# Kernel optimization log

Hardware: AMD Instinct MI355X
Metric: run time of the kernel (lower is better)

Reference implementation:

```python
import jax, jax.numpy as jnp
import numpy as np

D_MODEL = 1024
N_HEADS = 16
HEAD_DIM = D_MODEL // N_HEADS  # 64


def setup_inputs() -> dict:
    key = jax.random.key(0)
    k1, k2, k3 = jax.random.split(key, 3)
    x = jax.random.normal(k1, (2, 2048, D_MODEL), dtype=jnp.float32)
    # nn.Linear(d, 3d, bias=False): store transposed so y = x @ W
    w_qkv = jax.random.normal(k2, (D_MODEL, 3 * D_MODEL), dtype=jnp.float32) * (D_MODEL ** -0.5)
    w_proj = jax.random.normal(k3, (D_MODEL, D_MODEL), dtype=jnp.float32) * (D_MODEL ** -0.5)
    return {"x": x, "w_qkv": w_qkv, "w_proj": w_proj}


def reference(x, w_qkv, w_proj):
    b, n, _ = x.shape
    qkv = x @ w_qkv  # [b, n, 3*d_model]
    # einops 'b n (h d qkv) -> qkv b h n d': qkv axis is innermost of the split
    qkv = qkv.reshape(b, n, N_HEADS, HEAD_DIM, 3)
    q = jnp.moveaxis(qkv[..., 0], 1, 2)  # [b, h, n, d]
    k = jnp.moveaxis(qkv[..., 1], 1, 2)
    v = jnp.moveaxis(qkv[..., 2], 1, 2)
    scale = HEAD_DIM ** -0.5
    scores = jnp.einsum('bhqd,bhkd->bhqk', q, k) * scale  # [b, h, n, n]
    causal = jnp.tril(jnp.ones((n, n), dtype=bool))
    scores = jnp.where(causal[None, None], scores, -jnp.inf)
    attn = jax.nn.softmax(scores, axis=-1)
    out = jnp.einsum('bhqk,bhkd->bhqd', attn, v)  # [b, h, n, d]
    out = jnp.moveaxis(out, 1, 2).reshape(b, n, D_MODEL)  # 'b h n d -> b n (h d)'
    return out @ w_proj
```

## Files before the change

### kernel.cpp

```cpp
#include <hip/hip_runtime.h>
#include <cstdint>
#include <cstddef>

#define D_MODEL 1024
#define N_HEADS 16
#define HEAD_DIM 64
#define SEQ 2048
#define BATCH 2

typedef __attribute__((ext_vector_type(8))) short bf16x8;
typedef __attribute__((ext_vector_type(4))) float f32x4;

__device__ inline unsigned short f2bf(float f) {
    union { float f; unsigned u; } v; v.f = f;
    unsigned r = v.u + 0x7fffu + ((v.u >> 16) & 1u);
    return (unsigned short)(r >> 16);
}

__device__ __forceinline__ unsigned cvtpk_bf16(float lo, float hi) {
    unsigned r;
    asm("v_cvt_pk_bf16_f32 %0, %1, %2" : "=v"(r) : "v"(lo), "v"(hi));
    return r;
}
__device__ __forceinline__ unsigned short f2bf_hw(float f) {
    return (unsigned short)cvtpk_bf16(f, 0.f);
}

__device__ __forceinline__ void gload_lds16(const unsigned short* g, unsigned short* l) {
    __builtin_amdgcn_global_load_lds(
        (const __attribute__((address_space(1))) unsigned int*)g,
        (__attribute__((address_space(3))) unsigned int*)l, 16, 0, 0);
}

#define WAITCNT_VM4 0x0F74
#define WAITCNT_VM0 0x0F70

__global__ __launch_bounds__(256) void fused_convert_kernel(
    const float* __restrict__ X, unsigned short* __restrict__ Xb,
    const float* __restrict__ Wq, unsigned short* __restrict__ Wqt,
    const float* __restrict__ Wp, unsigned short* __restrict__ Wpt)
{
    const int blk = blockIdx.x;
    const int tid = threadIdx.x;
    __shared__ float t[32][33];

    if (blk < 2048) {
        const int idx = blk * 256 + tid;
        const float4* src = (const float4*)X;
        float4 v0 = src[idx * 2], v1 = src[idx * 2 + 1];
        uint4 o;
        o.x = cvtpk_bf16(v0.x, v0.y);
        o.y = cvtpk_bf16(v0.z, v0.w);
        o.z = cvtpk_bf16(v1.x, v1.y);
        o.w = cvtpk_bf16(v1.z, v1.w);
        ((uint4*)Xb)[idx] = o;
    } else if (blk < 5120) {
        const int bb = blk - 2048;
        const int c0 = (bb % 96) * 32, r0 = (bb / 96) * 32;
        const int a = tid & 31, b = tid >> 5;
#pragma unroll
        for (int i = 0; i < 32; i += 8)
            t[b + i][a] = Wq[(size_t)(r0 + b + i) * (3 * D_MODEL) + c0 + a];
        __syncthreads();
#pragma unroll
        for (int i = 0; i < 32; i += 8) {
            const int c = c0 + b + i;
            const int which = c % 3;
            const int np = which * 1024 + c / 3;
            const float s = (which == 0) ? 0.125f : 1.0f;
            Wqt[(size_t)np * D_MODEL + r0 + a] = f2bf_hw(t[a][b + i] * s);
        }
    } else {
        const int bb = blk - 5120;
        const int c0 = (bb % 32) * 32, r0 = (bb / 32) * 32;
        const int a = tid & 31, b = tid >> 5;
#pragma unroll
        for (int i = 0; i < 32; i += 8)
            t[b + i][a] = Wp[(size_t)(r0 + b + i) * D_MODEL + c0 + a];
        __syncthreads();
#pragma unroll
        for (int i = 0; i < 32; i += 8)
            Wpt[(size_t)(c0 + b + i) * D_MODEL + r0 + a] = f2bf_hw(t[a][b + i]);
    }
}

__global__ __launch_bounds__(256) void v_transpose(
    const unsigned short* __restrict__ V, unsigned short* __restrict__ Vt)
{
    const int n0 = blockIdx.x * 64;
    const int bh = blockIdx.y;
    __shared__ unsigned short t[64 * 72];
    const int tid = threadIdx.x;
    const uint4* src = (const uint4*)(V + ((size_t)bh * SEQ + n0) * HEAD_DIM);
#pragma unroll
    for (int it = 0; it < 2; it++) {
        const int lin = tid + it * 256;
        const int row = lin >> 3, p = lin & 7;
        ((uint4*)t)[row * 9 + p] = src[lin];
    }
    __syncthreads();
#pragma unroll
    for (int it = 0; it < 2; it++) {
        const int lin = tid + it * 256;
        const int drow = lin >> 3, p = lin & 7;
        union { unsigned short u[8]; uint4 v; } o;
#pragma unroll
        for (int e = 0; e < 8; e++) o.u[e] = t[(p * 8 + e) * 72 + drow];
        ((uint4*)(Vt + ((size_t)bh * HEAD_DIM + drow) * SEQ + n0))[p] = o.v;
    }
}

#define GEMM_PIPE3_BODY(A_, B_, KBASE, NITER, BX_, BY_)                        \
    const int tid = threadIdx.x;                                               \
    const int w = tid >> 6, lane = tid & 63;                                   \
    const int l15 = lane & 15, quad = lane >> 4;                               \
    const int wr = w >> 1, wc = w & 1;                                         \
    const int row0 = (BY_) * 128, col0 = (BX_) * 128;                          \
    __shared__ unsigned short As[3][4096];                                     \
    __shared__ unsigned short Bs[3][4096];                                     \
    const f32x4 zero4 = {0.f, 0.f, 0.f, 0.f};                                  \
    f32x4 acc[4][4];                                                           \
    _Pragma("unroll") for (int i = 0; i < 4; i++)                              \
        _Pragma("unroll") for (int j = 0; j < 4; j++) acc[i][j] = zero4;       \
    auto stage_ = [&](int sb_, int kt_) {                                      \
        const int k0 = (KBASE) + kt_ * 32 + quad * 8;                          \
        _Pragma("unroll") for (int i = 0; i < 2; i++) {                        \
            const int f = w * 2 + i;                                           \
            gload_lds16((A_) + (size_t)(row0 + f * 16 + l15) * D_MODEL + k0,   \
                        &As[sb_][f * 512 + lane * 8]);                         \
            gload_lds16((B_) + (size_t)(col0 + f * 16 + l15) * D_MODEL + k0,   \
                        &Bs[sb_][f * 512 + lane * 8]);                         \
        }                                                                      \
    };                                                                         \
    stage_(0, 0);                                                              \
    stage_(1, 1);                                                              \
    int sb = 0;                                                                \
    for (int kt = 0; kt < (NITER); kt++) {                                     \
        if (kt < (NITER) - 1) {                                                \
            __builtin_amdgcn_s_waitcnt(WAITCNT_VM4);                           \
            __builtin_amdgcn_s_barrier();                                      \
            if (kt + 2 < (NITER)) stage_((sb + 2 > 2) ? sb - 1 : sb + 2, kt + 2); \
        } else {                                                               \
            __builtin_amdgcn_s_waitcnt(WAITCNT_VM0);                           \
            __builtin_amdgcn_s_barrier();                                      \
        }                                                                      \
        bf16x8 af[4], bfr[4];                                                  \
        _Pragma("unroll") for (int i = 0; i < 4; i++)                          \
            af[i] = *(const bf16x8*)&As[sb][(wr * 4 + i) * 512 + lane * 8];    \
        _Pragma("unroll") for (int j = 0; j < 4; j++)                          \
            bfr[j] = *(const bf16x8*)&Bs[sb][(wc * 4 + j) * 512 + lane * 8];   \
        _Pragma("unroll") for (int i = 0; i < 4; i++)                          \
            _Pragma("unroll") for (int j = 0; j < 4; j++)                      \
                acc[i][j] = __builtin_amdgcn_mfma_f32_16x16x32_bf16(           \
                    af[i], bfr[j], acc[i][j], 0, 0, 0);                        \
        sb = (sb == 2) ? 0 : sb + 1;                                           \
    }

__global__ __launch_bounds__(256) void gemm_qkv_mfma(
    const unsigned short* __restrict__ A, const unsigned short* __restrict__ B,
    unsigned short* __restrict__ Q, unsigned short* __restrict__ Kq,
    unsigned short* __restrict__ Vb)
{
    const int lin = blockIdx.x + 24 * blockIdx.y;
    const int xcd = lin & 7, t = lin >> 3;
    const int bx = (xcd & 1) * 12 + t % 12;
    const int by = (xcd >> 1) * 8 + t / 12;
    GEMM_PIPE3_BODY(A, B, 0, 32, bx, by)
    const int nbase = col0 + wc * 64;
    const int which = nbase >> 10;
    unsigned short* const dst = (which == 0) ? Q : (which == 1) ? Kq : Vb;
#pragma unroll
    for (int i = 0; i < 4; i++) {
        const int rowb = row0 + wr * 64 + i * 16 + quad * 4;
        const int bb = rowb >> 11, n = rowb & (SEQ - 1);
#pragma unroll
        for (int rp = 0; rp < 2; rp++) {
#pragma unroll
            for (int j = 0; j < 4; j++) {
                const unsigned u = cvtpk_bf16(acc[i][j][2 * rp], acc[i][j][2 * rp + 1]);
                const int idx = (nbase + j * 16 + l15) & 1023;
                const int h = idx >> 6, dd = idx & 63;
                unsigned short* p =
                    dst + (((size_t)(bb * N_HEADS + h)) * SEQ + n + 2 * rp) * HEAD_DIM + dd;
                p[0] = (unsigned short)u;
                p[HEAD_DIM] = (unsigned short)(u >> 16);
            }
        }
    }
}

__global__ __launch_bounds__(256) void gemm_proj_splitk(
    const unsigned short* __restrict__ A, const unsigned short* __restrict__ B,
    float* __restrict__ P)
{
    const int lin = blockIdx.x + 8 * blockIdx.y;
    const int xcd = lin & 7, t = lin >> 3;
    const int bx = (xcd & 1) * 4 + t % 4;
    const int by = (xcd >> 1) * 8 + t / 4;
    const int kbase = blockIdx.z * 512;
    GEMM_PIPE3_BODY(A, B, kbase, 16, bx, by)
    float* const dst = P + (size_t)blockIdx.z * (4096ull * 1024ull);
#pragma unroll
    for (int i = 0; i < 4; i++) {
#pragma unroll
        for (int r = 0; r < 4; r++) {
            const int row = row0 + wr * 64 + i * 16 + quad * 4 + r;
#pragma unroll
            for (int j = 0; j < 4; j++) {
                const int c = col0 + wc * 64 + j * 16 + l15;
                dst[(size_t)row * D_MODEL + c] = acc[i][j][r];
            }
        }
    }
}

__global__ __launch_bounds__(256) void add_out_kernel(
    const float* __restrict__ P, float* __restrict__ out)
{
    const float4* p0 = (const float4*)P;
    const float4* p1 = (const float4*)(P + 4096ull * 1024ull);
    float4* o = (float4*)out;
    const int base = (blockIdx.x * 256 + threadIdx.x) * 4;
#pragma unroll
    for (int j = 0; j < 4; j++) {
        float4 a = p0[base + j], b = p1[base + j];
        float4 r = {a.x + b.x, a.y + b.y, a.z + b.z, a.w + b.w};
        o[base + j] = r;
    }
}

__global__ __launch_bounds__(256) void flash_attn_kernel(
    const unsigned short* __restrict__ Q,
    const unsigned short* __restrict__ K,
    const unsigned short* __restrict__ Vt,
    unsigned short* __restrict__ O)
{
    const int idx = blockIdx.x;
    const int bh = idx & 31;
    const int qt2 = idx >> 5;
    const int hi = qt2 >> 3, lo = qt2 & 7;
    const int qt = (hi == 0) ? lo : (hi == 1) ? 31 - lo : (hi == 2) ? lo + 8 : 23 - lo;

    const int tid = threadIdx.x;
    const int w = tid >> 6, lane = tid & 63;
    const int l15 = lane & 15, quad = lane >> 4;

    __shared__ unsigned short Ks[2][4096];
    __shared__ unsigned short Vs[2][4096];
    __shared__ unsigned short Ps[4][1024];

    bf16x8 qf[2];
    {
        const unsigned short* qrow =
            Q + ((size_t)bh * SEQ + qt * 64 + w * 16 + l15) * HEAD_DIM;
        qf[0] = *(const bf16x8*)(qrow + quad * 8);
        qf[1] = *(const bf16x8*)(qrow + 32 + quad * 8);
    }

    const f32x4 zero4 = {0.f, 0.f, 0.f, 0.f};
    f32x4 o_acc[4] = {zero4, zero4, zero4, zero4};
    float m_i = -1e30f, l_i = 0.f;

    auto stage = [&](int bf, int kt_t) {
        const int key0 = kt_t * 64;
#pragma unroll
        for (int i = 0; i < 2; i++) {
            const int f = w * 2 + i;
            const int ct = f >> 1, kh = f & 1;
            gload_lds16(K + ((size_t)bh * SEQ + key0 + ct * 16 + l15) * HEAD_DIM
                          + kh * 32 + quad * 8,
                        &Ks[bf][f * 512 + lane * 8]);
            gload_lds16(Vt + ((size_t)bh * HEAD_DIM + ct * 16 + l15) * SEQ
                           + key0 + kh * 32 + quad * 8,
                        &Vs[bf][f * 512 + lane * 8]);
        }
    };

    stage(0, 0);
    int buf = 0;

    const int qg = qt * 64 + w * 16 + l15;

    for (int kt = 0; kt <= qt; kt++) {
        __syncthreads();
        if (kt < qt) stage(buf ^ 1, kt + 1);

        f32x4 st[4] = {zero4, zero4, zero4, zero4};
        __builtin_amdgcn_s_setprio(1);
#pragma unroll
        for (int kh = 0; kh < 2; kh++) {
#pragma unroll
            for (int ct = 0; ct < 4; ct++) {
                bf16x8 kf = *(const bf16x8*)&Ks[buf][(ct * 2 + kh) * 512 + lane * 8];
                st[ct] = __builtin_amdgcn_mfma_f32_16x16x32_bf16(kf, qf[kh], st[ct], 0, 0, 0);
            }
        }
        __builtin_amdgcn_s_setprio(0);

        float mt = -1e30f;
        if (kt == qt) {
#pragma unroll
            for (int ct = 0; ct < 4; ct++) {
#pragma unroll
                for (int r = 0; r < 4; r++) {
                    const int kg = kt * 64 + ct * 16 + quad * 4 + r;
                    float v = (kg > qg) ? -1e30f : st[ct][r];
                    st[ct][r] = v;
                    mt = fmaxf(mt, v);
                }
            }
        } else {
#pragma unroll
            for (int ct = 0; ct < 4; ct++)
#pragma unroll
                for (int r = 0; r < 4; r++)
                    mt = fmaxf(mt, st[ct][r]);
        }
        mt = fmaxf(mt, __shfl_xor(mt, 16));
        mt = fmaxf(mt, __shfl_xor(mt, 32));

        float mn = m_i;
        if (!__all(mt <= m_i + 8.0f)) {
            mn = fmaxf(m_i, mt);
            const float alpha = __expf(m_i - mn);
            m_i = mn;
            l_i *= alpha;
            float ar[4];
#pragma unroll
            for (int r = 0; r < 4; r++)
                ar[r] = __shfl(alpha, (lane & 48) | (quad * 4 + r));
#pragma unroll
            for (int dt = 0; dt < 4; dt++)
#pragma unroll
                for (int r = 0; r < 4; r++)
                    o_acc[dt][r] *= ar[r];
        }

        float ls = 0.f;
#pragma unroll
        for (int ct = 0; ct < 4; ct++) {
            const float p0 = __expf(st[ct][0] - mn);
            const float p1 = __expf(st[ct][1] - mn);
            const float p2 = __expf(st[ct][2] - mn);
            const float p3 = __expf(st[ct][3] - mn);
            ls += (p0 + p1) + (p2 + p3);
            uint2 pk2;
            pk2.x = cvtpk_bf16(p0, p1);
            pk2.y = cvtpk_bf16(p2, p3);
            const int addr = (ct >> 1) * 512 + ((ct & 1) * 2 + (quad >> 1)) * 128
                           + l15 * 8 + (quad & 1) * 4;
            *(uint2*)&Ps[w][addr] = pk2;
        }
        l_i += ls;

        __builtin_amdgcn_s_setprio(1);
#pragma unroll
        for (int kh = 0; kh < 2; kh++) {
            bf16x8 pa = *(const bf16x8*)&Ps[w][kh * 512 + quad * 128 + l15 * 8];
#pragma unroll
            for (int dt = 0; dt < 4; dt++) {
                bf16x8 vf = *(const bf16x8*)&Vs[buf][(dt * 2 + kh) * 512 + lane * 8];
                o_acc[dt] = __builtin_amdgcn_mfma_f32_16x16x32_bf16(pa, vf, o_acc[dt], 0, 0, 0);
            }
        }
        __builtin_amdgcn_s_setprio(0);
        buf ^= 1;
    }

    l_i += __shfl_xor(l_i, 16);
    l_i += __shfl_xor(l_i, 32);
    const float linv = 1.0f / l_i;
    float lr[4];
#pragma unroll
    for (int r = 0; r < 4; r++)
        lr[r] = __shfl(linv, (lane & 48) | (quad * 4 + r));

    const int b = bh >> 4, h = bh & 15;
#pragma unroll
    for (int r = 0; r < 4; r++) {
        const int q = qt * 64 + w * 16 + quad * 4 + r;
        unsigned short* orow = O + ((size_t)b * SEQ + q) * D_MODEL + h * HEAD_DIM;
#pragma unroll
        for (int dt = 0; dt < 4; dt++)
            orow[dt * 16 + l15] = f2bf_hw(o_acc[dt][r] * lr[r]);
    }
}

extern "C" void kernel_launch(void* const* d_in, const int* in_sizes, int n_in,
                              void* d_out, int out_size, void* d_ws, size_t ws_size,
                              hipStream_t stream) {
    const float* x      = (const float*)d_in[0];
    const float* w_qkv  = (const float*)d_in[1];
    const float* w_proj = (const float*)d_in[2];
    float* out = (float*)d_out;

    unsigned short* Xb  = (unsigned short*)d_ws;
    unsigned short* Wqt = Xb  + (size_t)4 * 1024 * 1024;
    unsigned short* Wpt = Wqt + (size_t)3 * 1024 * 1024;
    unsigned short* Qb  = Wpt + (size_t)1 * 1024 * 1024;
    unsigned short* Kb  = Qb  + (size_t)4 * 1024 * 1024;
    unsigned short* Vb  = Kb  + (size_t)4 * 1024 * 1024;
    unsigned short* Vtb = Vb  + (size_t)4 * 1024 * 1024;
    unsigned short* Ob  = Vtb + (size_t)4 * 1024 * 1024;

    float* Pp = (float*)Qb;

    fused_convert_kernel<<<dim3(6144), 256, 0, stream>>>(
        x, Xb, w_qkv, Wqt, w_proj, Wpt);

    gemm_qkv_mfma<<<dim3(3 * D_MODEL / 128, BATCH * SEQ / 128), 256, 0, stream>>>(
        Xb, Wqt, Qb, Kb, Vb);

    v_transpose<<<dim3(SEQ / 64, BATCH * N_HEADS), 256, 0, stream>>>(Vb, Vtb);

    flash_attn_kernel<<<dim3(SEQ / 64 * BATCH * N_HEADS), 256, 0, stream>>>(
        Qb, Kb, Vtb, Ob);

    gemm_proj_splitk<<<dim3(D_MODEL / 128, BATCH * SEQ / 128, 2), 256, 0, stream>>>(
        Ob, Wpt, Pp);

    add_out_kernel<<<dim3(1024), 256, 0, stream>>>(Pp, out);
}
```

Measured before the change: 216.2 us.

## Fuse V transpose into QKV GEMM epilogue and raise MFMA wave priority

The QKV GEMM epilogue now writes the V columns straight into the transposed [b,h,d,n] layout as packed 32-bit stores, so the separate v_transpose kernel and its extra read/write pass over V are removed. It also wraps the MFMA block in s_setprio(1)/s_setprio(0) so waves issuing matrix ops get scheduling priority over waves that are loading. The transposed stores are strided by SEQ across lanes and so coalesce less well, which may slow the epilogue.

```diff
diff --git a/kernel.cpp b/kernel.cpp
--- a/kernel.cpp
+++ b/kernel.cpp
@@ -81,32 +81,6 @@
 #pragma unroll
         for (int i = 0; i < 32; i += 8)
             Wpt[(size_t)(c0 + b + i) * D_MODEL + r0 + a] = f2bf_hw(t[a][b + i]);
-    }
-}
-
-__global__ __launch_bounds__(256) void v_transpose(
-    const unsigned short* __restrict__ V, unsigned short* __restrict__ Vt)
-{
-    const int n0 = blockIdx.x * 64;
-    const int bh = blockIdx.y;
-    __shared__ unsigned short t[64 * 72];
-    const int tid = threadIdx.x;
-    const uint4* src = (const uint4*)(V + ((size_t)bh * SEQ + n0) * HEAD_DIM);
-#pragma unroll
-    for (int it = 0; it < 2; it++) {
-        const int lin = tid + it * 256;
-        const int row = lin >> 3, p = lin & 7;
-        ((uint4*)t)[row * 9 + p] = src[lin];
-    }
-    __syncthreads();
-#pragma unroll
-    for (int it = 0; it < 2; it++) {
-        const int lin = tid + it * 256;
-        const int drow = lin >> 3, p = lin & 7;
-        union { unsigned short u[8]; uint4 v; } o;
-#pragma unroll
-        for (int e = 0; e < 8; e++) o.u[e] = t[(p * 8 + e) * 72 + drow];
-        ((uint4*)(Vt + ((size_t)bh * HEAD_DIM + drow) * SEQ + n0))[p] = o.v;
     }
 }
 
@@ -149,17 +123,19 @@
             af[i] = *(const bf16x8*)&As[sb][(wr * 4 + i) * 512 + lane * 8];    \
         _Pragma("unroll") for (int j = 0; j < 4; j++)                          \
             bfr[j] = *(const bf16x8*)&Bs[sb][(wc * 4 + j) * 512 + lane * 8];   \
+        __builtin_amdgcn_s_setprio(1);                                         \
         _Pragma("unroll") for (int i = 0; i < 4; i++)                          \
             _Pragma("unroll") for (int j = 0; j < 4; j++)                      \
                 acc[i][j] = __builtin_amdgcn_mfma_f32_16x16x32_bf16(           \
                     af[i], bfr[j], acc[i][j], 0, 0, 0);                        \
+        __builtin_amdgcn_s_setprio(0);                                         \
         sb = (sb == 2) ? 0 : sb + 1;                                           \
     }
 
 __global__ __launch_bounds__(256) void gemm_qkv_mfma(
     const unsigned short* __restrict__ A, const unsigned short* __restrict__ B,
     unsigned short* __restrict__ Q, unsigned short* __restrict__ Kq,
-    unsigned short* __restrict__ Vb)
+    unsigned short* __restrict__ Vt)
 {
     const int lin = blockIdx.x + 24 * blockIdx.y;
     const int xcd = lin & 7, t = lin >> 3;
@@ -168,22 +144,40 @@
     GEMM_PIPE3_BODY(A, B, 0, 32, bx, by)
     const int nbase = col0 + wc * 64;
     const int which = nbase >> 10;
-    unsigned short* const dst = (which == 0) ? Q : (which == 1) ? Kq : Vb;
-#pragma unroll
-    for (int i = 0; i < 4; i++) {
-        const int rowb = row0 + wr * 64 + i * 16 + quad * 4;
-        const int bb = rowb >> 11, n = rowb & (SEQ - 1);
-#pragma unroll
-        for (int rp = 0; rp < 2; rp++) {
-#pragma unroll
-            for (int j = 0; j < 4; j++) {
-                const unsigned u = cvtpk_bf16(acc[i][j][2 * rp], acc[i][j][2 * rp + 1]);
-                const int idx = (nbase + j * 16 + l15) & 1023;
-                const int h = idx >> 6, dd = idx & 63;
-                unsigned short* p =
-                    dst + (((size_t)(bb * N_HEADS + h)) * SEQ + n + 2 * rp) * HEAD_DIM + dd;
-                p[0] = (unsigned short)u;
-                p[HEAD_DIM] = (unsigned short)(u >> 16);
+    if (which < 2) {
+        unsigned short* const dst = (which == 0) ? Q : Kq;
+#pragma unroll
+        for (int i = 0; i < 4; i++) {
+            const int rowb = row0 + wr * 64 + i * 16 + quad * 4;
+            const int bb = rowb >> 11, n = rowb & (SEQ - 1);
+#pragma unroll
+            for (int rp = 0; rp < 2; rp++) {
+#pragma unroll
+                for (int j = 0; j < 4; j++) {
+                    const unsigned u = cvtpk_bf16(acc[i][j][2 * rp], acc[i][j][2 * rp + 1]);
+                    const int idx = (nbase + j * 16 + l15) & 1023;
+                    const int h = idx >> 6, dd = idx & 63;
+                    unsigned short* p =
+                        dst + (((size_t)(bb * N_HEADS + h)) * SEQ + n + 2 * rp) * HEAD_DIM + dd;
+                    p[0] = (unsigned short)u;
+                    p[HEAD_DIM] = (unsigned short)(u >> 16);
+                }
+            }
+        }
+    } else {
+#pragma unroll
+        for (int i = 0; i < 4; i++) {
+            const int rowb = row0 + wr * 64 + i * 16 + quad * 4;
+            const int bb = rowb >> 11, n = rowb & (SEQ - 1);
+#pragma unroll
+            for (int rp = 0; rp < 2; rp++) {
+#pragma unroll
+                for (int j = 0; j < 4; j++) {
+                    const unsigned u = cvtpk_bf16(acc[i][j][2 * rp], acc[i][j][2 * rp + 1]);
+                    const int idx = (nbase + j * 16 + l15) & 1023;
+                    *(unsigned*)&Vt[((size_t)(bb * N_HEADS + (idx >> 6)) * HEAD_DIM
+                                     + (idx & 63)) * SEQ + n + 2 * rp] = u;
+                }
             }
         }
     }
@@ -409,9 +403,7 @@
         x, Xb, w_qkv, Wqt, w_proj, Wpt);
 
     gemm_qkv_mfma<<<dim3(3 * D_MODEL / 128, BATCH * SEQ / 128), 256, 0, stream>>>(
-        Xb, Wqt, Qb, Kb, Vb);
-
-    v_transpose<<<dim3(SEQ / 64, BATCH * N_HEADS), 256, 0, stream>>>(Vb, Vtb);
+        Xb, Wqt, Qb, Kb, Vtb);
 
     flash_attn_kernel<<<dim3(SEQ / 64 * BATCH * N_HEADS), 256, 0, stream>>>(
         Qb, Kb, Vtb, Ob);
```

Result: no change. 212.2 us (-1.9%).
